# Kernel tuning notes

Hardware: AMD Instinct MI355X
Metric: run time of the kernel (lower is better)

## Reference

```python
import jax, jax.numpy as jnp
import numpy as np

N_NODES = 50000
HIDDEN = 128
N_REL = 9
N_LAYERS = 3
N_EDGES = 600000


def setup_inputs() -> dict:
    key = jax.random.key(0)
    k1, k2, k3, k4, k5 = jax.random.split(key, 5)
    edge_index = jax.random.randint(k1, (2, N_EDGES), 0, N_NODES, dtype=jnp.int64 if jax.config.jax_enable_x64 else jnp.int32)
    edge_type = jax.random.randint(k2, (N_EDGES,), 0, N_REL, dtype=edge_index.dtype)
    embeddings = jax.random.uniform(k3, (N_NODES, HIDDEN), dtype=jnp.float32)
    weights = jax.random.uniform(k4, (N_LAYERS, N_REL, HIDDEN, HIDDEN), dtype=jnp.float32)
    biases = jax.random.uniform(k5, (N_LAYERS, N_REL, HIDDEN), dtype=jnp.float32)
    return {"edge_index": edge_index, "edge_type": edge_type,
            "embeddings": embeddings, "weights": weights, "biases": biases}


def reference(edge_index, edge_type, embeddings, weights, biases):
    # RGCN: per relation r, messages = emb[src] @ W[l,r] + b[l,r], scatter-summed
    # into dest. Equivalent vectorized form: precompute X = emb @ W for all
    # relations ([R,N,E]), then a single gather + segment_sum over edges.
    L = weights.shape[0]
    N = embeddings.shape[0]
    dest = edge_index[0]
    src = edge_index[1]
    out = embeddings
    for l in range(L):
        X = jnp.einsum('ne,ref->rnf', out, weights[l])        # [R, N, E]
        msg = X[edge_type, src] + biases[l][edge_type]        # [num_edges, E]
        hidden = jax.ops.segment_sum(msg, dest, num_segments=N)  # [N, E]
        if l + 1 < L:
            hidden = jax.nn.relu(hidden)
        out = hidden
    return out
```

## Files before the change

kernel.cpp:

```cpp
#include <hip/hip_runtime.h>

#define NNODES 50000
#define HID 128
#define NREL 9
#define NLAYERS 3
#define NEDGES 600000

#define NBINS (NREL * NNODES)
#define SCAN_CHUNK 1024
#define NBLK ((NBINS + SCAN_CHUNK - 1) / SCAN_CHUNK)

#define KTOT (NREL * HID)
#define GM2 32
#define FPITCH 136

#define HIST_BLKS ((NEDGES + 255) / 256)
#define EMB_BLKS  ((NNODES * HID / 8) / 256)
#define W_BLKS    (NLAYERS * NREL)

typedef __attribute__((ext_vector_type(8))) short short8;
typedef __attribute__((ext_vector_type(4))) float f32x4;

__device__ __forceinline__ short f2bf(float f) {
    union { float f; unsigned u; } c; c.f = f;
    unsigned r = c.u + 0x7fff + ((c.u >> 16) & 1);
    return (short)(r >> 16);
}
__device__ __forceinline__ float bf2f(short v) {
    return __uint_as_float(((unsigned)(unsigned short)v) << 16);
}


__global__ __launch_bounds__(256) void prep_kernel(const int* __restrict__ dst,
                                                   const int* __restrict__ etype,
                                                   int* __restrict__ bins,
                                                   const float* __restrict__ E,
                                                   short* __restrict__ Ebf,
                                                   const float* __restrict__ W,
                                                   short* __restrict__ Wt2) {
    int b = blockIdx.x, tid = threadIdx.x;
    if (b < HIST_BLKS) {
        int e = b * 256 + tid;
        if (e < NEDGES) {
            int bin = etype[e] * NNODES + dst[e];
            atomicAdd(&bins[bin], 1);
        }
    } else if (b < HIST_BLKS + EMB_BLKS) {
        int gid = (b - HIST_BLKS) * 256 + tid;
        const float* p = E + (size_t)gid * 8;
        float4 v0 = *(const float4*)p;
        float4 v1 = *(const float4*)(p + 4);
        short8 o = {f2bf(v0.x), f2bf(v0.y), f2bf(v0.z), f2bf(v0.w),
                    f2bf(v1.x), f2bf(v1.y), f2bf(v1.z), f2bf(v1.w)};
        *(short8*)(Ebf + (size_t)gid * 8) = o;
    } else {
        int lr = b - HIST_BLKS - EMB_BLKS;
        int l = lr / NREL, r = lr - l * NREL;
        const float* w = W + (size_t)lr * HID * HID;
        short* o = Wt2 + (size_t)l * HID * KTOT;
#pragma unroll 4
        for (int i = 0; i < 64; i++) {
            int elem = i * 256 + tid;
            int kk = elem >> 7, n = elem & 127;
            o[(size_t)n * KTOT + r * HID + kk] = f2bf(w[elem]);
        }
    }
}


__global__ __launch_bounds__(256) void scan_pass1(const int* __restrict__ bins,
                                                  int* __restrict__ blocksum) {
    __shared__ int red[256];
    int b = blockIdx.x, t = threadIdx.x;
    int i0 = b * SCAN_CHUNK + t * 4;
    int s = 0;
#pragma unroll
    for (int k = 0; k < 4; k++)
        if (i0 + k < NBINS) s += bins[i0 + k];
    red[t] = s;
    __syncthreads();
    for (int off = 128; off > 0; off >>= 1) {
        if (t < off) red[t] += red[t + off];
        __syncthreads();
    }
    if (t == 0) blocksum[b] = red[0];
}

__global__ __launch_bounds__(512) void scan_pass2(const int* __restrict__ blocksum,
                                                  int* __restrict__ blockoff,
                                                  int* __restrict__ rowptr) {
    __shared__ int s[512];
    int t = threadIdx.x;
    int v = (t < NBLK) ? blocksum[t] : 0;
    s[t] = v;
    __syncthreads();
    for (int off = 1; off < 512; off <<= 1) {
        int x = (t >= off) ? s[t - off] : 0;
        __syncthreads();
        s[t] += x;
        __syncthreads();
    }
    if (t < NBLK) blockoff[t] = s[t] - v;
    if (t == 0) rowptr[NBINS] = NEDGES;
}

__global__ __launch_bounds__(256) void scan_pass3(const int* __restrict__ bins,
                                                  const int* __restrict__ blockoff,
                                                  int* __restrict__ rowptr,
                                                  int* __restrict__ cursor) {
    __shared__ int sc[256];
    int b = blockIdx.x, t = threadIdx.x;
    int i0 = b * SCAN_CHUNK + t * 4;
    int v[4], p[4];
    int s = 0;
#pragma unroll
    for (int k = 0; k < 4; k++) {
        v[k] = (i0 + k < NBINS) ? bins[i0 + k] : 0;
        p[k] = s;
        s += v[k];
    }
    sc[t] = s;
    __syncthreads();
    for (int off = 1; off < 256; off <<= 1) {
        int x = (t >= off) ? sc[t - off] : 0;
        __syncthreads();
        sc[t] += x;
        __syncthreads();
    }
    int base = blockoff[b] + (sc[t] - s);
#pragma unroll
    for (int k = 0; k < 4; k++) {
        if (i0 + k < NBINS) {
            rowptr[i0 + k] = base + p[k];
            cursor[i0 + k] = base + p[k];
        }
    }
}

__global__ void place_kernel(const int* __restrict__ dst, const int* __restrict__ src,
                             const int* __restrict__ etype,
                             int* __restrict__ cursor, int* __restrict__ bsrc) {
    int e = blockIdx.x * blockDim.x + threadIdx.x;
    if (e < NEDGES) {
        int bin = etype[e] * NNODES + dst[e];
        int pos = atomicAdd(&cursor[bin], 1);
        bsrc[pos] = src[e];
    }
}


__global__ __launch_bounds__(256, 4) void fused_kernel(const short* __restrict__ Hin,
                                                       const short* __restrict__ Wt2l,
                                                       const float* __restrict__ Bias,
                                                       const int* __restrict__ rowptr,
                                                       const int* __restrict__ bsrc,
                                                       short* __restrict__ HoutBf,
                                                       float* __restrict__ HoutF,
                                                       int last) {
    __shared__ short As[2][GM2 * FPITCH];
    __shared__ int   rp_s[NREL * (GM2 + 1)];
    __shared__ float bias_s[NREL * HID];

    int tid  = threadIdx.x;
    int wave = tid >> 6, lane = tid & 63;
    int lm = lane & 15, lq = lane >> 4;
    int row0 = blockIdx.x * GM2;
    int n0   = wave * 32;
    int grow = tid >> 3;
    int gcc  = tid & 7;

    int d0  = row0 + grow;
    int dc  = (d0     > NNODES) ? NNODES : d0;
    int dc1 = (d0 + 1 > NNODES) ? NNODES : (d0 + 1);
    int rs0 = rowptr[dc];
    int re0 = rowptr[dc1];
    int pf0 = 0, pf1 = 0, pf2 = 0, pf3 = 0;
    if (rs0 < re0) {
        pf0 = bsrc[rs0];
        pf1 = bsrc[rs0 + 1];
        pf2 = bsrc[rs0 + 2];
        pf3 = bsrc[rs0 + 3];
    }

    for (int i = tid; i < NREL * (GM2 + 1); i += 256) {
        int r = i / (GM2 + 1), o = i - r * (GM2 + 1);
        int d = row0 + o; if (d > NNODES) d = NNODES;
        rp_s[i] = rowptr[r * NNODES + d];
    }
    for (int i = tid; i < NREL * HID; i += 256) bias_s[i] = Bias[i];

    f32x4 acc[2][2];
#pragma unroll
    for (int a = 0; a < 2; a++)
#pragma unroll
        for (int b = 0; b < 2; b++) acc[a][b] = (f32x4){0.f, 0.f, 0.f, 0.f};

    __syncthreads();

    const short* wb = Wt2l + (size_t)(n0 + lm) * KTOT + lq * 8;
    const short* hb = Hin + gcc * 16;

    for (int r = 0; r < NREL; r++) {
        short* Ap = &As[r & 1][0];

        short8 bfr[2][4];
#pragma unroll
        for (int nt = 0; nt < 2; nt++)
#pragma unroll
            for (int ks = 0; ks < 4; ks++)
                bfr[nt][ks] = *(const short8*)(wb + (size_t)nt * 16 * KTOT + r * HID + ks * 32);

        int rs = rp_s[r * (GM2 + 1) + grow];
        int re = rp_s[r * (GM2 + 1) + grow + 1];
        float ga[16];
#pragma unroll
        for (int i = 0; i < 16; i++) ga[i] = 0.f;

        int j = rs;
        if (j < re) {
            int rem = re - j;
            int s0 = pf0;
            int s1 = (rem > 1) ? pf1 : s0;
            int s2 = (rem > 2) ? pf2 : s0;
            int s3 = (rem > 3) ? pf3 : s0;
            const short8* p0 = (const short8*)(hb + (size_t)s0 * HID);
            const short8* p1 = (const short8*)(hb + (size_t)s1 * HID);
            const short8* p2 = (const short8*)(hb + (size_t)s2 * HID);
            const short8* p3 = (const short8*)(hb + (size_t)s3 * HID);
            short8 a0 = p0[0], a1 = p0[1];
            short8 b0 = p1[0], b1 = p1[1];
            short8 c0 = p2[0], c1 = p2[1];
            short8 d0v = p3[0], d1v = p3[1];
            float m1 = (rem > 1) ? 1.f : 0.f;
            float m2 = (rem > 2) ? 1.f : 0.f;
            float m3 = (rem > 3) ? 1.f : 0.f;
#pragma unroll
            for (int k = 0; k < 8; k++) {
                ga[k]     += (bf2f(a0[k]) + m1 * bf2f(b0[k])) + (m2 * bf2f(c0[k]) + m3 * bf2f(d0v[k]));
                ga[k + 8] += (bf2f(a1[k]) + m1 * bf2f(b1[k])) + (m2 * bf2f(c1[k]) + m3 * bf2f(d1v[k]));
            }
            j += 4;
        }
        for (; j < re; j += 4) {
            int rem = re - j;
            int s0 = bsrc[j];
            int t1 = bsrc[j + 1];
            int t2 = bsrc[j + 2];
            int t3 = bsrc[j + 3];
            int s1 = (rem > 1) ? t1 : s0;
            int s2 = (rem > 2) ? t2 : s0;
            int s3 = (rem > 3) ? t3 : s0;
            const short8* p0 = (const short8*)(hb + (size_t)s0 * HID);
            const short8* p1 = (const short8*)(hb + (size_t)s1 * HID);
            const short8* p2 = (const short8*)(hb + (size_t)s2 * HID);
            const short8* p3 = (const short8*)(hb + (size_t)s3 * HID);
            short8 a0 = p0[0], a1 = p0[1];
            short8 b0 = p1[0], b1 = p1[1];
            short8 c0 = p2[0], c1 = p2[1];
            short8 d0v = p3[0], d1v = p3[1];
            float m1 = (rem > 1) ? 1.f : 0.f;
            float m2 = (rem > 2) ? 1.f : 0.f;
            float m3 = (rem > 3) ? 1.f : 0.f;
#pragma unroll
            for (int k = 0; k < 8; k++) {
                ga[k]     += (bf2f(a0[k]) + m1 * bf2f(b0[k])) + (m2 * bf2f(c0[k]) + m3 * bf2f(d0v[k]));
                ga[k + 8] += (bf2f(a1[k]) + m1 * bf2f(b1[k])) + (m2 * bf2f(c1[k]) + m3 * bf2f(d1v[k]));
            }
        }

        {
            short8 o0, o1;
#pragma unroll
            for (int i = 0; i < 8; i++) {
                o0[i] = f2bf(ga[i]);
                o1[i] = f2bf(ga[i + 8]);
            }
            short8* ap = (short8*)&Ap[grow * FPITCH + gcc * 16];
            ap[0] = o0; ap[1] = o1;
        }

        if (r + 1 < NREL) {
            int nrs = rp_s[(r + 1) * (GM2 + 1) + grow];
            int nre = rp_s[(r + 1) * (GM2 + 1) + grow + 1];
            if (nrs < nre) {
                pf0 = bsrc[nrs];
                pf1 = bsrc[nrs + 1];
                pf2 = bsrc[nrs + 2];
                pf3 = bsrc[nrs + 3];
            }
        }
        __syncthreads();

#pragma unroll
        for (int ks = 0; ks < 4; ks++) {
            short8 af0 = *(const short8*)&Ap[(lm     ) * FPITCH + ks * 32 + lq * 8];
            short8 af1 = *(const short8*)&Ap[(lm + 16) * FPITCH + ks * 32 + lq * 8];
            __builtin_amdgcn_s_setprio(1);
            acc[0][0] = __builtin_amdgcn_mfma_f32_16x16x32_bf16(af0, bfr[0][ks], acc[0][0], 0, 0, 0);
            acc[1][0] = __builtin_amdgcn_mfma_f32_16x16x32_bf16(af1, bfr[0][ks], acc[1][0], 0, 0, 0);
            acc[0][1] = __builtin_amdgcn_mfma_f32_16x16x32_bf16(af0, bfr[1][ks], acc[0][1], 0, 0, 0);
            acc[1][1] = __builtin_amdgcn_mfma_f32_16x16x32_bf16(af1, bfr[1][ks], acc[1][1], 0, 0, 0);
            __builtin_amdgcn_s_setprio(0);
        }
    }

    __syncthreads();

    if (!last) {
        short (*Et)[FPITCH] = (short(*)[FPITCH])&As[0][0];
#pragma unroll
        for (int mt = 0; mt < 2; mt++) {
#pragma unroll
            for (int reg = 0; reg < 4; reg++) {
                int rl = mt * 16 + lq * 4 + reg;
                float cr[NREL];
#pragma unroll
                for (int rr = 0; rr < NREL; rr++)
                    cr[rr] = (float)(rp_s[rr * (GM2 + 1) + rl + 1] - rp_s[rr * (GM2 + 1) + rl]);
#pragma unroll
                for (int nt = 0; nt < 2; nt++) {
                    int n = n0 + nt * 16 + lm;
                    float b = 0.f;
#pragma unroll
                    for (int rr = 0; rr < NREL; rr++) b += cr[rr] * bias_s[rr * HID + n];
                    float o = fmaxf(acc[mt][nt][reg] + b, 0.f);
                    Et[rl][n] = f2bf(o);
                }
            }
        }
        __syncthreads();
#pragma unroll
        for (int i = 0; i < 2; i++) {
            int p = i * 256 + tid;
            int row = p >> 4, cc = p & 15;
            int d = row0 + row;
            if (d < NNODES)
                *(short8*)(HoutBf + (size_t)d * HID + cc * 8) = *(const short8*)&Et[row][cc * 8];
        }
    } else {
#pragma unroll
        for (int mt = 0; mt < 2; mt++) {
#pragma unroll
            for (int reg = 0; reg < 4; reg++) {
                int rl = mt * 16 + lq * 4 + reg;
                int d  = row0 + rl;
                if (d >= NNODES) continue;
                float cr[NREL];
#pragma unroll
                for (int rr = 0; rr < NREL; rr++)
                    cr[rr] = (float)(rp_s[rr * (GM2 + 1) + rl + 1] - rp_s[rr * (GM2 + 1) + rl]);
#pragma unroll
                for (int nt = 0; nt < 2; nt++) {
                    int n = n0 + nt * 16 + lm;
                    float b = 0.f;
#pragma unroll
                    for (int rr = 0; rr < NREL; rr++) b += cr[rr] * bias_s[rr * HID + n];
                    HoutF[(size_t)d * HID + n] = acc[mt][nt][reg] + b;
                }
            }
        }
    }
}


extern "C" void kernel_launch(void* const* d_in, const int* in_sizes, int n_in,
                              void* d_out, int out_size, void* d_ws, size_t ws_size,
                              hipStream_t stream) {
    const int*   edge_index = (const int*)d_in[0];
    const int*   etype      = (const int*)d_in[1];
    const float* emb        = (const float*)d_in[2];
    const float* W          = (const float*)d_in[3];
    const float* Bias       = (const float*)d_in[4];
    float*       out        = (float*)d_out;

    const int* dst  = edge_index;
    const int* srcA = edge_index + NEDGES;

    short* Ebf  = (short*)d_ws;
    short* HbfA = Ebf  + (size_t)NNODES * HID;
    short* HbfB = HbfA + (size_t)NNODES * HID;
    short* Wt2  = HbfB + (size_t)NNODES * HID;
    int*   bsrc     = (int*)(Wt2 + (size_t)NLAYERS * HID * KTOT);
    int*   bins     = bsrc + NEDGES + 8;
    int*   cursor   = bins + NBINS;
    int*   rowptr   = cursor + NBINS;
    int*   blocksum = rowptr + NBINS + 1;
    int*   blockoff = blocksum + NBLK;

    hipMemsetAsync(bins, 0, NBINS * sizeof(int), stream);
    prep_kernel<<<HIST_BLKS + EMB_BLKS + W_BLKS, 256, 0, stream>>>(
        dst, etype, bins, emb, Ebf, W, Wt2);
    scan_pass1<<<NBLK, 256, 0, stream>>>(bins, blocksum);
    scan_pass2<<<1, 512, 0, stream>>>(blocksum, blockoff, rowptr);
    scan_pass3<<<NBLK, 256, 0, stream>>>(bins, blockoff, rowptr, cursor);
    place_kernel<<<(NEDGES + 255) / 256, 256, 0, stream>>>(dst, srcA, etype, cursor, bsrc);

    const int nblocks = (NNODES + GM2 - 1) / GM2;
    const short* Hin = Ebf;
    for (int l = 0; l < NLAYERS; l++) {
        int last = (l + 1 == NLAYERS);
        short* Hout = (l == 0) ? HbfA : HbfB;
        if (l == 2) Hout = HbfA;
        const short* Wtl = Wt2 + (size_t)l * HID * KTOT;
        const float* Bl  = Bias + (size_t)l * NREL * HID;
        fused_kernel<<<nblocks, 256, 0, stream>>>(
            Hin, Wtl, Bl, rowptr, bsrc, Hout, out, last);
        Hin = Hout;
    }
}
```

Baseline: 438.7 us.

## Split fused gather+GEMM into separate gather kernel and GEMM kernel per layer

The fused per-layer kernel is split into two kernels. A gather kernel aggregates the bf16 neighbor rows per relation into a materialized [N, 9*128] bf16 buffer, parallelised over 64-row tiles and 4 column slices. A GEMM kernel then streams that buffer through LDS into MFMA. The aim is more parallelism and memory-level overlap for the irregular gather, which previously stalled the MFMA pipeline. The cost is writing and re-reading a ~115MB intermediate per layer, plus an extra launch.

```diff
diff --git a/kernel.cpp b/kernel.cpp
--- a/kernel.cpp
+++ b/kernel.cpp
@@ -13,6 +13,11 @@
 #define KTOT (NREL * HID)
 #define GM2 32
 #define FPITCH 136
+
+#define GSLICES 4
+#define GCOLS 32
+#define GROWS 64
+#define GTILES ((NNODES + GROWS - 1) / GROWS)
 
 #define HIST_BLKS ((NEDGES + 255) / 256)
 #define EMB_BLKS  ((NNODES * HID / 8) / 256)
@@ -149,72 +154,39 @@
 }
 
 
-__global__ __launch_bounds__(256, 4) void fused_kernel(const short* __restrict__ Hin,
-                                                       const short* __restrict__ Wt2l,
-                                                       const float* __restrict__ Bias,
-                                                       const int* __restrict__ rowptr,
-                                                       const int* __restrict__ bsrc,
-                                                       short* __restrict__ HoutBf,
-                                                       float* __restrict__ HoutF,
-                                                       int last) {
-    __shared__ short As[2][GM2 * FPITCH];
-    __shared__ int   rp_s[NREL * (GM2 + 1)];
-    __shared__ float bias_s[NREL * HID];
-
-    int tid  = threadIdx.x;
-    int wave = tid >> 6, lane = tid & 63;
-    int lm = lane & 15, lq = lane >> 4;
-    int row0 = blockIdx.x * GM2;
-    int n0   = wave * 32;
-    int grow = tid >> 3;
-    int gcc  = tid & 7;
-
-    int d0  = row0 + grow;
-    int dc  = (d0     > NNODES) ? NNODES : d0;
-    int dc1 = (d0 + 1 > NNODES) ? NNODES : (d0 + 1);
-    int rs0 = rowptr[dc];
-    int re0 = rowptr[dc1];
-    int pf0 = 0, pf1 = 0, pf2 = 0, pf3 = 0;
-    if (rs0 < re0) {
-        pf0 = bsrc[rs0];
-        pf1 = bsrc[rs0 + 1];
-        pf2 = bsrc[rs0 + 2];
-        pf3 = bsrc[rs0 + 3];
-    }
-
-    for (int i = tid; i < NREL * (GM2 + 1); i += 256) {
-        int r = i / (GM2 + 1), o = i - r * (GM2 + 1);
+__global__ __launch_bounds__(256) void gather_kernel(const short* __restrict__ Hin,
+                                                     const int* __restrict__ rowptr,
+                                                     const int* __restrict__ bsrc,
+                                                     short* __restrict__ S) {
+    __shared__ int rp_s[NREL * (GROWS + 1)];
+    int bid = blockIdx.x;
+    int slice = bid & (GSLICES - 1);
+    int tile  = bid >> 2;
+    int row0  = tile * GROWS;
+    int tid   = threadIdx.x;
+    int grow  = tid >> 2;
+    int lc    = tid & 3;
+
+    for (int i = tid; i < NREL * (GROWS + 1); i += 256) {
+        int r = i / (GROWS + 1), o = i - r * (GROWS + 1);
         int d = row0 + o; if (d > NNODES) d = NNODES;
         rp_s[i] = rowptr[r * NNODES + d];
     }
-    for (int i = tid; i < NREL * HID; i += 256) bias_s[i] = Bias[i];
-
-    f32x4 acc[2][2];
-#pragma unroll
-    for (int a = 0; a < 2; a++)
-#pragma unroll
-        for (int b = 0; b < 2; b++) acc[a][b] = (f32x4){0.f, 0.f, 0.f, 0.f};
-
-    __syncthreads();
-
-    const short* wb = Wt2l + (size_t)(n0 + lm) * KTOT + lq * 8;
-    const short* hb = Hin + gcc * 16;
+    __syncthreads();
+
+    const short* hb = Hin + slice * GCOLS + lc * 8;
+    short*       sp = S + (size_t)(row0 + grow) * KTOT + slice * GCOLS + lc * 8;
+    int active = (row0 + grow) < NNODES;
+
+    int rs = rp_s[grow];
+    int re = rp_s[grow + 1];
+    int pf0 = 0, pf1 = 0, pf2 = 0, pf3 = 0;
+    if (rs < re) { pf0 = bsrc[rs]; pf1 = bsrc[rs + 1]; pf2 = bsrc[rs + 2]; pf3 = bsrc[rs + 3]; }
 
     for (int r = 0; r < NREL; r++) {
-        short* Ap = &As[r & 1][0];
-
-        short8 bfr[2][4];
-#pragma unroll
-        for (int nt = 0; nt < 2; nt++)
-#pragma unroll
-            for (int ks = 0; ks < 4; ks++)
-                bfr[nt][ks] = *(const short8*)(wb + (size_t)nt * 16 * KTOT + r * HID + ks * 32);
-
-        int rs = rp_s[r * (GM2 + 1) + grow];
-        int re = rp_s[r * (GM2 + 1) + grow + 1];
-        float ga[16];
-#pragma unroll
-        for (int i = 0; i < 16; i++) ga[i] = 0.f;
+        float ga[8];
+#pragma unroll
+        for (int i = 0; i < 8; i++) ga[i] = 0.f;
 
         int j = rs;
         if (j < re) {
@@ -223,22 +195,16 @@
             int s1 = (rem > 1) ? pf1 : s0;
             int s2 = (rem > 2) ? pf2 : s0;
             int s3 = (rem > 3) ? pf3 : s0;
-            const short8* p0 = (const short8*)(hb + (size_t)s0 * HID);
-            const short8* p1 = (const short8*)(hb + (size_t)s1 * HID);
-            const short8* p2 = (const short8*)(hb + (size_t)s2 * HID);
-            const short8* p3 = (const short8*)(hb + (size_t)s3 * HID);
-            short8 a0 = p0[0], a1 = p0[1];
-            short8 b0 = p1[0], b1 = p1[1];
-            short8 c0 = p2[0], c1 = p2[1];
-            short8 d0v = p3[0], d1v = p3[1];
+            short8 a = *(const short8*)(hb + (size_t)s0 * HID);
+            short8 b = *(const short8*)(hb + (size_t)s1 * HID);
+            short8 c = *(const short8*)(hb + (size_t)s2 * HID);
+            short8 d = *(const short8*)(hb + (size_t)s3 * HID);
             float m1 = (rem > 1) ? 1.f : 0.f;
             float m2 = (rem > 2) ? 1.f : 0.f;
             float m3 = (rem > 3) ? 1.f : 0.f;
 #pragma unroll
-            for (int k = 0; k < 8; k++) {
-                ga[k]     += (bf2f(a0[k]) + m1 * bf2f(b0[k])) + (m2 * bf2f(c0[k]) + m3 * bf2f(d0v[k]));
-                ga[k + 8] += (bf2f(a1[k]) + m1 * bf2f(b1[k])) + (m2 * bf2f(c1[k]) + m3 * bf2f(d1v[k]));
-            }
+            for (int k = 0; k < 8; k++)
+                ga[k] += (bf2f(a[k]) + m1 * bf2f(b[k])) + (m2 * bf2f(c[k]) + m3 * bf2f(d[k]));
             j += 4;
         }
         for (; j < re; j += 4) {
@@ -250,44 +216,89 @@
             int s1 = (rem > 1) ? t1 : s0;
             int s2 = (rem > 2) ? t2 : s0;
             int s3 = (rem > 3) ? t3 : s0;
-            const short8* p0 = (const short8*)(hb + (size_t)s0 * HID);
-            const short8* p1 = (const short8*)(hb + (size_t)s1 * HID);
-            const short8* p2 = (const short8*)(hb + (size_t)s2 * HID);
-            const short8* p3 = (const short8*)(hb + (size_t)s3 * HID);
-            short8 a0 = p0[0], a1 = p0[1];
-            short8 b0 = p1[0], b1 = p1[1];
-            short8 c0 = p2[0], c1 = p2[1];
-            short8 d0v = p3[0], d1v = p3[1];
+            short8 a = *(const short8*)(hb + (size_t)s0 * HID);
+            short8 b = *(const short8*)(hb + (size_t)s1 * HID);
+            short8 c = *(const short8*)(hb + (size_t)s2 * HID);
+            short8 d = *(const short8*)(hb + (size_t)s3 * HID);
             float m1 = (rem > 1) ? 1.f : 0.f;
             float m2 = (rem > 2) ? 1.f : 0.f;
             float m3 = (rem > 3) ? 1.f : 0.f;
 #pragma unroll
-            for (int k = 0; k < 8; k++) {
-                ga[k]     += (bf2f(a0[k]) + m1 * bf2f(b0[k])) + (m2 * bf2f(c0[k]) + m3 * bf2f(d0v[k]));
-                ga[k + 8] += (bf2f(a1[k]) + m1 * bf2f(b1[k])) + (m2 * bf2f(c1[k]) + m3 * bf2f(d1v[k]));
-            }
-        }
-
-        {
-            short8 o0, o1;
-#pragma unroll
-            for (int i = 0; i < 8; i++) {
-                o0[i] = f2bf(ga[i]);
-                o1[i] = f2bf(ga[i + 8]);
-            }
-            short8* ap = (short8*)&Ap[grow * FPITCH + gcc * 16];
-            ap[0] = o0; ap[1] = o1;
+            for (int k = 0; k < 8; k++)
+                ga[k] += (bf2f(a[k]) + m1 * bf2f(b[k])) + (m2 * bf2f(c[k]) + m3 * bf2f(d[k]));
         }
 
         if (r + 1 < NREL) {
-            int nrs = rp_s[(r + 1) * (GM2 + 1) + grow];
-            int nre = rp_s[(r + 1) * (GM2 + 1) + grow + 1];
-            if (nrs < nre) {
-                pf0 = bsrc[nrs];
-                pf1 = bsrc[nrs + 1];
-                pf2 = bsrc[nrs + 2];
-                pf3 = bsrc[nrs + 3];
-            }
+            rs = rp_s[(r + 1) * (GROWS + 1) + grow];
+            re = rp_s[(r + 1) * (GROWS + 1) + grow + 1];
+            if (rs < re) { pf0 = bsrc[rs]; pf1 = bsrc[rs + 1]; pf2 = bsrc[rs + 2]; pf3 = bsrc[rs + 3]; }
+        }
+
+        short8 o;
+#pragma unroll
+        for (int k = 0; k < 8; k++) o[k] = f2bf(ga[k]);
+        if (active) *(short8*)(sp + r * HID) = o;
+    }
+}
+
+
+__global__ __launch_bounds__(256, 4) void gemm_kernel(const short* __restrict__ S,
+                                                      const short* __restrict__ Wt2l,
+                                                      const float* __restrict__ Bias,
+                                                      const int* __restrict__ rowptr,
+                                                      short* __restrict__ HoutBf,
+                                                      float* __restrict__ HoutF,
+                                                      int last) {
+    __shared__ short As[2][GM2 * FPITCH];
+    __shared__ int   rp_s[NREL * (GM2 + 1)];
+    __shared__ float bias_s[NREL * HID];
+
+    int tid  = threadIdx.x;
+    int wave = tid >> 6, lane = tid & 63;
+    int lm = lane & 15, lq = lane >> 4;
+    int row0 = blockIdx.x * GM2;
+    int n0   = wave * 32;
+    int grow = tid >> 3;
+    int gcc  = tid & 7;
+
+    for (int i = tid; i < NREL * (GM2 + 1); i += 256) {
+        int r = i / (GM2 + 1), o = i - r * (GM2 + 1);
+        int d = row0 + o; if (d > NNODES) d = NNODES;
+        rp_s[i] = rowptr[r * NNODES + d];
+    }
+    for (int i = tid; i < NREL * HID; i += 256) bias_s[i] = Bias[i];
+
+    int ar = row0 + grow; if (ar > NNODES - 1) ar = NNODES - 1;
+    const short* sb = S + (size_t)ar * KTOT + gcc * 16;
+
+    short8 ra0 = *(const short8*)(sb);
+    short8 ra1 = *(const short8*)(sb + 8);
+
+    f32x4 acc[2][2];
+#pragma unroll
+    for (int a = 0; a < 2; a++)
+#pragma unroll
+        for (int b = 0; b < 2; b++) acc[a][b] = (f32x4){0.f, 0.f, 0.f, 0.f};
+
+    const short* wb = Wt2l + (size_t)(n0 + lm) * KTOT + lq * 8;
+
+    __syncthreads();
+
+    for (int kc = 0; kc < NREL; kc++) {
+        short* Ap = &As[kc & 1][0];
+
+        short8 bfr[2][4];
+#pragma unroll
+        for (int nt = 0; nt < 2; nt++)
+#pragma unroll
+            for (int ks = 0; ks < 4; ks++)
+                bfr[nt][ks] = *(const short8*)(wb + (size_t)nt * 16 * KTOT + kc * HID + ks * 32);
+
+        short8* ap = (short8*)&Ap[grow * FPITCH + gcc * 16];
+        ap[0] = ra0; ap[1] = ra1;
+        if (kc + 1 < NREL) {
+            ra0 = *(const short8*)(sb + (kc + 1) * HID);
+            ra1 = *(const short8*)(sb + (kc + 1) * HID + 8);
         }
         __syncthreads();
 
@@ -303,7 +314,6 @@
             __builtin_amdgcn_s_setprio(0);
         }
     }
-
     __syncthreads();
 
     if (!last) {
@@ -378,8 +388,8 @@
 
     short* Ebf  = (short*)d_ws;
     short* HbfA = Ebf  + (size_t)NNODES * HID;
-    short* HbfB = HbfA + (size_t)NNODES * HID;
-    short* Wt2  = HbfB + (size_t)NNODES * HID;
+    short* S    = HbfA + (size_t)NNODES * HID;
+    short* Wt2  = S + (size_t)NNODES * KTOT;
     int*   bsrc     = (int*)(Wt2 + (size_t)NLAYERS * HID * KTOT);
     int*   bins     = bsrc + NEDGES + 8;
     int*   cursor   = bins + NBINS;
@@ -395,16 +405,14 @@
     scan_pass3<<<NBLK, 256, 0, stream>>>(bins, blockoff, rowptr, cursor);
     place_kernel<<<(NEDGES + 255) / 256, 256, 0, stream>>>(dst, srcA, etype, cursor, bsrc);
 
-    const int nblocks = (NNODES + GM2 - 1) / GM2;
+    const int gemm_blocks = (NNODES + GM2 - 1) / GM2;
     const short* Hin = Ebf;
     for (int l = 0; l < NLAYERS; l++) {
         int last = (l + 1 == NLAYERS);
-        short* Hout = (l == 0) ? HbfA : HbfB;
-        if (l == 2) Hout = HbfA;
         const short* Wtl = Wt2 + (size_t)l * HID * KTOT;
         const float* Bl  = Bias + (size_t)l * NREL * HID;
-        fused_kernel<<<nblocks, 256, 0, stream>>>(
-            Hin, Wtl, Bl, rowptr, bsrc, Hout, out, last);
-        Hin = Hout;
-    }
-}
+        gather_kernel<<<GTILES * GSLICES, 256, 0, stream>>>(Hin, rowptr, bsrc, S);
+        gemm_kernel<<<gemm_blocks, 256, 0, stream>>>(S, Wtl, Bl, rowptr, HbfA, out, last);
+        Hin = HbfA;
+    }
+}
```

Result: slower. 535.4 us (+22.0%).
